# Kernel tuning notes

Measured on AMD Instinct MI355X. Metric: run time of the kernel, lower is better.

## Reference

```python
import jax, jax.numpy as jnp
import numpy as np

N_CHANNELS = 512
GROUPS = 8
EPS = 1e-5


def setup_inputs() -> dict:
    key = jax.random.key(0)
    ks = jax.random.split(key, 7)
    B, C, L = 8, N_CHANNELS, 4096
    s = 1.0 / np.sqrt(C)
    return {
        "x": jax.random.normal(ks[0], (B, C, L), dtype=jnp.float32),
        "gamma": jnp.ones((C,), dtype=jnp.float32),
        "beta": jnp.zeros((C,), dtype=jnp.float32),
        "w_qkv": jax.random.normal(ks[1], (3 * C, C), dtype=jnp.float32) * s,
        "b_qkv": jax.random.normal(ks[2], (3 * C,), dtype=jnp.float32) * 0.01,
        "w_out": jax.random.normal(ks[3], (C, C), dtype=jnp.float32) * s,
        "b_out": jax.random.normal(ks[4], (C,), dtype=jnp.float32) * 0.01,
    }


def group_norm(x, gamma, beta):
    # x: [B, C, L]; normalize per group of C//GROUPS channels over (channels_in_group, L)
    B, C, L = x.shape
    xg = x.reshape(B, GROUPS, C // GROUPS, L)
    mean = xg.mean(axis=(2, 3), keepdims=True)
    var = xg.var(axis=(2, 3), keepdims=True)
    xn = ((xg - mean) * jax.lax.rsqrt(var + EPS)).reshape(B, C, L)
    return xn * gamma[None, :, None] + beta[None, :, None]


def reference(x, gamma, beta, w_qkv, b_qkv, w_out, b_out):
    B, C, L = x.shape
    xn = group_norm(x, gamma, beta)
    # 1x1 conv == channel matmul: [3C, C] @ [B, C, L] -> [B, 3C, L]
    qkv = jnp.einsum('oc,bcl->bol', w_qkv, xn) + b_qkv[None, :, None]
    q, k, v = jnp.split(qkv, 3, axis=1)  # each [B, C, L]
    scale = C ** (-0.5)
    attn = jnp.einsum('bcl,bck->blk', q, k) * scale  # [B, L, L]
    attn = jax.nn.softmax(attn, axis=-1)
    out = jnp.einsum('blk,bck->bcl', attn, v)  # [B, C, L]
    proj = jnp.einsum('oc,bcl->bol', w_out, out) + b_out[None, :, None]
    return x + proj
```

## Files before the change

### kernel.cpp

```cpp
#include <hip/hip_runtime.h>

typedef __attribute__((ext_vector_type(4))) float f32x4;
typedef __attribute__((ext_vector_type(8))) short short8;
typedef unsigned short u16;
typedef unsigned int u32;

static constexpr int Bb = 8, Cc = 512, Ll = 4096;

__device__ __forceinline__ u16 f2bf(float f) {
  u32 u = __builtin_bit_cast(u32, f);
  u = (u + 0x7FFFu + ((u >> 16) & 1u)) >> 16;
  return (u16)u;
}

__device__ __forceinline__ void load_lds16(const void* g, void* l) {
  __builtin_amdgcn_global_load_lds((const __attribute__((address_space(1))) void*)g,
                                   (__attribute__((address_space(3))) void*)l,
                                   16, 0, 0);
}

__global__ void cvt_bf16_kernel(const float* __restrict__ src, u16* __restrict__ dst, int n) {
  int stride = gridDim.x * blockDim.x;
  for (int i = blockIdx.x * blockDim.x + threadIdx.x; i < n; i += stride)
    dst[i] = f2bf(src[i]);
}

__global__ __launch_bounds__(256)
void gn_stats_kernel(const float* __restrict__ x, float* __restrict__ stats) {
  int bg = blockIdx.x;
  const f32x4* p = (const f32x4*)(x + (size_t)bg * (64 * Ll));
  float s = 0.f, ss = 0.f;
  for (int i = threadIdx.x; i < 64 * Ll / 4; i += 256) {
    f32x4 v = p[i];
    s  += v[0] + v[1] + v[2] + v[3];
    ss += v[0]*v[0] + v[1]*v[1] + v[2]*v[2] + v[3]*v[3];
  }
  __shared__ float rs[256], rq[256];
  rs[threadIdx.x] = s; rq[threadIdx.x] = ss;
  __syncthreads();
  for (int st = 128; st > 0; st >>= 1) {
    if (threadIdx.x < st) { rs[threadIdx.x] += rs[threadIdx.x + st]; rq[threadIdx.x] += rq[threadIdx.x + st]; }
    __syncthreads();
  }
  if (threadIdx.x == 0) {
    const float inv_n = 1.f / (64.f * 4096.f);
    float mean = rs[0] * inv_n;
    float var  = rq[0] * inv_n - mean * mean;
    stats[bg * 2]     = mean;
    stats[bg * 2 + 1] = rsqrtf(var + 1e-5f);
  }
}

__global__ __launch_bounds__(256)
void gn_apply_t_kernel(const float* __restrict__ x, const float* __restrict__ gamma,
                       const float* __restrict__ beta, const float* __restrict__ stats,
                       u16* __restrict__ xn_t) {
  int lt = blockIdx.x;
  int ct = blockIdx.y;
  int b  = blockIdx.z;
  __shared__ float tile[64][65];
  int t = threadIdx.x;
  int lx = t & 63;
  int qd = t >> 6;
  int c0 = ct * 64, l0 = lt * 64;
  float mean = stats[(b * 8 + ct) * 2];
  float rstd = stats[(b * 8 + ct) * 2 + 1];
  #pragma unroll
  for (int i = 0; i < 16; ++i) {
    int cl = qd + i * 4;
    int c = c0 + cl;
    float v = x[((size_t)b * Cc + c) * Ll + l0 + lx];
    tile[cl][lx] = (v - mean) * rstd * gamma[c] + beta[c];
  }
  __syncthreads();
  #pragma unroll
  for (int i = 0; i < 16; ++i) {
    int ll = qd + i * 4;
    xn_t[((size_t)b * Ll + l0 + ll) * Cc + c0 + lx] = f2bf(tile[lx][ll]);
  }
}

template <int MODE>
__global__ __launch_bounds__(256, 2)
void gemm_tn(const u16* __restrict__ A, long long aStride, int lda,
             const u16* __restrict__ Bm, long long bStride, int ldb,
             void* __restrict__ Dv, long long dStride, int ldd,
             const float* __restrict__ bias, const float* __restrict__ resid, int K) {
  int z = blockIdx.z;
  A  += (size_t)z * aStride;
  Bm += (size_t)z * bStride;
  int m0 = blockIdx.x * 128, n0 = blockIdx.y * 128;
  __shared__ uint4 sA[1024], sB[1024];
  int tid = threadIdx.x, lane = tid & 63;
  int wv = tid >> 6, wr = wv >> 1, wc = wv & 1;
  int l15 = lane & 15, l4 = lane >> 4;
  f32x4 acc[4][4] = {};
  for (int kt = 0; kt < K; kt += 64) {
    __syncthreads();
    #pragma unroll
    for (int p = 0; p < 4; ++p) {
      int slot = p * 256 + tid;
      int r = slot >> 3, g = slot & 7, gw = g ^ (r & 7);
      load_lds16(A  + (size_t)(m0 + r) * lda + kt + gw * 8, &sA[slot]);
      load_lds16(Bm + (size_t)(n0 + r) * ldb + kt + gw * 8, &sB[slot]);
    }
    __syncthreads();
    #pragma unroll
    for (int ks = 0; ks < 2; ++ks) {
      short8 af[4], bfr[4];
      #pragma unroll
      for (int i = 0; i < 4; ++i) {
        int ra = 64 * wr + 16 * i + l15;
        af[i]  = *(const short8*)&sA[ra * 8 + ((4 * ks + l4) ^ (ra & 7))];
        int rb = 64 * wc + 16 * i + l15;
        bfr[i] = *(const short8*)&sB[rb * 8 + ((4 * ks + l4) ^ (rb & 7))];
      }
      #pragma unroll
      for (int i = 0; i < 4; ++i)
        #pragma unroll
        for (int j = 0; j < 4; ++j)
          acc[i][j] = __builtin_amdgcn_mfma_f32_16x16x32_bf16(af[i], bfr[j], acc[i][j], 0, 0, 0);
    }
  }
  #pragma unroll
  for (int i = 0; i < 4; ++i) {
    #pragma unroll
    for (int j = 0; j < 4; ++j) {
      #pragma unroll
      for (int r = 0; r < 4; ++r) {
        int m = m0 + 64 * wr + 16 * i + 4 * l4 + r;
        int n = n0 + 64 * wc + 16 * j + l15;
        float val = acc[i][j][r] + (MODE == 0 ? bias[n] : bias[m]);
        size_t idx = (size_t)z * dStride + (size_t)m * ldd + n;
        if (MODE == 2) ((float*)Dv)[idx] = val + resid[idx];
        else           ((u16*)Dv)[idx]   = f2bf(val);
      }
    }
  }
}

__global__ __launch_bounds__(512, 2)
void flash_attn_kernel(const u16* __restrict__ qk_t, const u16* __restrict__ v,
                       u16* __restrict__ o_t) {
  int b  = blockIdx.y;
  int q0 = blockIdx.x * 128;
  int tid = threadIdx.x, lane = tid & 63, wv = tid >> 6;
  int l15 = lane & 15, l4 = lane >> 4;
  const u16* qkb = qk_t + (size_t)b * Ll * 1024;
  const u16* vb  = v    + (size_t)b * Cc * Ll;
  u16* ob        = o_t  + (size_t)b * Ll * Cc;

  __shared__ uint4 sK[2][32 * 64];
  __shared__ uint4 sV[2][512 * 4];
  __shared__ __align__(16) char sP[128 * 80];
  __shared__ __align__(16) float sAl[128];

  int ow_q = wv >> 2, ow_c = wv & 3;

  short8 aq[16];
  {
    const u16* qp = qkb + (size_t)(q0 + wv * 16 + l15) * 1024 + 8 * l4;
    #pragma unroll
    for (int ks = 0; ks < 16; ++ks) aq[ks] = *(const short8*)(qp + 32 * ks);
  }

  auto issueK = [&](int kt, int buf) {
    #pragma unroll
    for (int p = 0; p < 4; ++p) {
      int slot = p * 512 + tid;
      int r = slot >> 6, g = slot & 63, gw = g ^ (r & 7);
      load_lds16(qkb + (size_t)(kt * 32 + r) * 1024 + 512 + gw * 8, &sK[buf][slot]);
    }
  };
  auto issueV = [&](int kt, int buf) {
    #pragma unroll
    for (int p = 0; p < 4; ++p) {
      int slot = p * 512 + tid;
      int r = slot >> 2, g = slot & 3, gw = g ^ ((r >> 1) & 3);
      load_lds16(vb + (size_t)r * Ll + kt * 32 + gw * 8, &sV[buf][slot]);
    }
  };
  issueK(0, 0);
  issueV(0, 0);

  f32x4 accO[4][8];
  #pragma unroll
  for (int i = 0; i < 4; ++i)
    #pragma unroll
    for (int j = 0; j < 8; ++j) accO[i][j] = (f32x4){0.f, 0.f, 0.f, 0.f};
  float mrun = -1e30f, lrun = 0.f;
  const float scale = 0.044194173824159216f;

  const int NT = Ll / 32;
  for (int kt = 0; kt < NT; ++kt) {
    int buf = kt & 1;
    __syncthreads();
    if (kt + 1 < NT) { issueK(kt + 1, buf ^ 1); issueV(kt + 1, buf ^ 1); }

    const uint4* kb = &sK[buf][0];
    f32x4 s2[2];
    #pragma unroll
    for (int t = 0; t < 2; ++t) {
      s2[t] = (f32x4){0.f, 0.f, 0.f, 0.f};
      int krow = 16 * t + l15;
      #pragma unroll
      for (int ks = 0; ks < 16; ++ks) {
        short8 ak = *(const short8*)&kb[krow * 64 + ((4 * ks + l4) ^ (krow & 7))];
        s2[t] = __builtin_amdgcn_mfma_f32_16x16x32_bf16(ak, aq[ks], s2[t], 0, 0, 0);
      }
    }

    #pragma unroll
    for (int t = 0; t < 2; ++t)
      #pragma unroll
      for (int r = 0; r < 4; ++r) s2[t][r] *= scale;
    float mx = fmaxf(fmaxf(s2[0][0], s2[0][1]), fmaxf(s2[0][2], s2[0][3]));
    mx = fmaxf(mx, fmaxf(fmaxf(s2[1][0], s2[1][1]), fmaxf(s2[1][2], s2[1][3])));
    mx = fmaxf(mx, __shfl_xor(mx, 16));
    mx = fmaxf(mx, __shfl_xor(mx, 32));
    float mnew = fmaxf(mrun, mx);
    float al = __expf(mrun - mnew);
    mrun = mnew;
    float ps = 0.f;
    #pragma unroll
    for (int t = 0; t < 2; ++t)
      #pragma unroll
      for (int r = 0; r < 4; ++r) { float pv = __expf(s2[t][r] - mnew); s2[t][r] = pv; ps += pv; }
    ps += __shfl_xor(ps, 16);
    ps += __shfl_xor(ps, 32);
    lrun = lrun * al + ps;

    {
      char* pb = sP + (16 * wv + l15) * 80;
      #pragma unroll
      for (int t = 0; t < 2; ++t) {
        u32 lo = (u32)f2bf(s2[t][0]) | ((u32)f2bf(s2[t][1]) << 16);
        u32 hi = (u32)f2bf(s2[t][2]) | ((u32)f2bf(s2[t][3]) << 16);
        uint2 w = {lo, hi};
        *(uint2*)(pb + 32 * t + 8 * l4) = w;
      }
      if (lane < 16) sAl[16 * wv + lane] = al;
    }

    __builtin_amdgcn_sched_barrier(0);
    asm volatile("s_waitcnt lgkmcnt(0)" ::: "memory");
    __builtin_amdgcn_s_barrier();
    __builtin_amdgcn_sched_barrier(0);

    #pragma unroll
    for (int i = 0; i < 4; ++i) {
      f32x4 av = *(const f32x4*)&sAl[64 * ow_q + 16 * i + 4 * l4];
      #pragma unroll
      for (int j = 0; j < 8; ++j) {
        #pragma unroll
        for (int r = 0; r < 4; ++r) accO[i][j][r] *= av[r];
      }
    }
    short8 ap[4];
    #pragma unroll
    for (int i = 0; i < 4; ++i) {
      int ra = 64 * ow_q + 16 * i + l15;
      ap[i] = *(const short8*)(sP + ra * 80 + 16 * l4);
    }
    const uint4* vbuf = &sV[buf][0];
    #pragma unroll
    for (int j = 0; j < 8; ++j) {
      int crow = 128 * ow_c + 16 * j + l15;
      short8 bv = *(const short8*)&vbuf[crow * 4 + (l4 ^ ((crow >> 1) & 3))];
      #pragma unroll
      for (int i = 0; i < 4; ++i)
        accO[i][j] = __builtin_amdgcn_mfma_f32_16x16x32_bf16(ap[i], bv, accO[i][j], 0, 0, 0);
    }
  }

  __syncthreads();
  if (lane < 16) sAl[16 * wv + lane] = lrun;
  __syncthreads();
  #pragma unroll
  for (int i = 0; i < 4; ++i) {
    f32x4 lv = *(const f32x4*)&sAl[64 * ow_q + 16 * i + 4 * l4];
    #pragma unroll
    for (int r = 0; r < 4; ++r) lv[r] = 1.f / lv[r];
    #pragma unroll
    for (int j = 0; j < 8; ++j) {
      #pragma unroll
      for (int r = 0; r < 4; ++r) {
        int q = q0 + 64 * ow_q + 16 * i + 4 * l4 + r;
        int c = 128 * ow_c + 16 * j + l15;
        ob[(size_t)q * Cc + c] = f2bf(accO[i][j][r] * lv[r]);
      }
    }
  }
}

extern "C" void kernel_launch(void* const* d_in, const int* in_sizes, int n_in,
                              void* d_out, int out_size, void* d_ws, size_t ws_size,
                              hipStream_t stream) {
  const float* x     = (const float*)d_in[0];
  const float* gamma = (const float*)d_in[1];
  const float* beta  = (const float*)d_in[2];
  const float* w_qkv = (const float*)d_in[3];
  const float* b_qkv = (const float*)d_in[4];
  const float* w_out = (const float*)d_in[5];
  const float* b_out = (const float*)d_in[6];
  float* out = (float*)d_out;

  char* ws = (char*)d_ws;
  size_t off = 0;
  auto alloc = [&](size_t bytes) -> char* {
    char* p = ws + off;
    off += (bytes + 1023) & ~(size_t)1023;
    return p;
  };
  float* stats = (float*)alloc(64 * 2 * sizeof(float));
  u16* wqb = (u16*)alloc((size_t)1536 * 512 * 2);
  u16* wob = (u16*)alloc((size_t)512 * 512 * 2);
  u16* xnt = (u16*)alloc((size_t)Bb * Ll * Cc * 2);
  u16* qkt = (u16*)alloc((size_t)Bb * Ll * 1024 * 2);
  u16* vbf = (u16*)alloc((size_t)Bb * Cc * Ll * 2);
  u16* ot  = xnt;
  if (off > ws_size) return;

  cvt_bf16_kernel<<<256, 256, 0, stream>>>(w_qkv, wqb, 1536 * 512);
  cvt_bf16_kernel<<<256, 256, 0, stream>>>(w_out, wob, 512 * 512);
  gn_stats_kernel<<<64, 256, 0, stream>>>(x, stats);
  gn_apply_t_kernel<<<dim3(64, 8, 8), 256, 0, stream>>>(x, gamma, beta, stats, xnt);
  gemm_tn<0><<<dim3(32, 8, 8), 256, 0, stream>>>(
      xnt, (long long)Ll * Cc, Cc, wqb, 0, Cc,
      qkt, (long long)Ll * 1024, 1024, b_qkv, nullptr, Cc);
  gemm_tn<1><<<dim3(4, 32, 8), 256, 0, stream>>>(
      wqb + (size_t)1024 * 512, 0, Cc, xnt, (long long)Ll * Cc, Cc,
      vbf, (long long)Cc * Ll, Ll, b_qkv + 1024, nullptr, Cc);
  flash_attn_kernel<<<dim3(32, 8), 512, 0, stream>>>(qkt, vbf, ot);
  gemm_tn<2><<<dim3(4, 32, 8), 256, 0, stream>>>(
      wob, 0, Cc, ot, (long long)Ll * Cc, Cc,
      out, (long long)Cc * Ll, Ll, b_out, x, Cc);
}
```

Measured before the change: 745.8 us.

## Replace XOR-swizzled LDS layouts with fragment-ordered tiles and interleave attention blocks across batches

The GEMM and flash-attention K tiles are now stored in LDS in MFMA fragment order instead of an XOR-swizzled row layout, so each wave's fragment reads hit contiguous addresses. This targets LDS bank conflicts and address arithmetic in the inner loops. The P scratch buffer row stride drops from 80 to 64 bytes, which may bring back bank conflicts on the P writes and reads. The attention grid is flattened so consecutive blocks cycle through batches, which changes how work and L2 traffic spread across CUs.

```diff
diff --git a/kernel.cpp b/kernel.cpp
--- a/kernel.cpp
+++ b/kernel.cpp
@@ -99,10 +99,11 @@
     __syncthreads();
     #pragma unroll
     for (int p = 0; p < 4; ++p) {
-      int slot = p * 256 + tid;
-      int r = slot >> 3, g = slot & 7, gw = g ^ (r & 7);
-      load_lds16(A  + (size_t)(m0 + r) * lda + kt + gw * 8, &sA[slot]);
-      load_lds16(Bm + (size_t)(n0 + r) * ldb + kt + gw * 8, &sB[slot]);
+      int s = p * 256 + tid;
+      int r = ((s >> 7) << 4) | (((s >> 2) & 1) << 3) | ((s >> 3) & 7);
+      int g = (((s >> 6) & 1) << 2) | (s & 3);
+      load_lds16(A  + (size_t)(m0 + r) * lda + kt + g * 8, &sA[s]);
+      load_lds16(Bm + (size_t)(n0 + r) * ldb + kt + g * 8, &sB[s]);
     }
     __syncthreads();
     #pragma unroll
@@ -110,10 +111,10 @@
       short8 af[4], bfr[4];
       #pragma unroll
       for (int i = 0; i < 4; ++i) {
-        int ra = 64 * wr + 16 * i + l15;
-        af[i]  = *(const short8*)&sA[ra * 8 + ((4 * ks + l4) ^ (ra & 7))];
-        int rb = 64 * wc + 16 * i + l15;
-        bfr[i] = *(const short8*)&sB[rb * 8 + ((4 * ks + l4) ^ (rb & 7))];
+        int sa = (4 * wr + i) * 128 + ks * 64 + (l15 & 7) * 8 + (l15 >> 3) * 4 + l4;
+        af[i]  = *(const short8*)&sA[sa];
+        int sb = (4 * wc + i) * 128 + ks * 64 + (l15 & 7) * 8 + (l15 >> 3) * 4 + l4;
+        bfr[i] = *(const short8*)&sB[sb];
       }
       #pragma unroll
       for (int i = 0; i < 4; ++i)
@@ -142,8 +143,9 @@
 __global__ __launch_bounds__(512, 2)
 void flash_attn_kernel(const u16* __restrict__ qk_t, const u16* __restrict__ v,
                        u16* __restrict__ o_t) {
-  int b  = blockIdx.y;
-  int q0 = blockIdx.x * 128;
+  int bid = blockIdx.x;
+  int b  = bid & 7;
+  int q0 = (bid >> 3) * 128;
   int tid = threadIdx.x, lane = tid & 63, wv = tid >> 6;
   int l15 = lane & 15, l4 = lane >> 4;
   const u16* qkb = qk_t + (size_t)b * Ll * 1024;
@@ -152,7 +154,7 @@
 
   __shared__ uint4 sK[2][32 * 64];
   __shared__ uint4 sV[2][512 * 4];
-  __shared__ __align__(16) char sP[128 * 80];
+  __shared__ __align__(16) char sP[128 * 64];
   __shared__ __align__(16) float sAl[128];
 
   int ow_q = wv >> 2, ow_c = wv & 3;
@@ -167,17 +169,18 @@
   auto issueK = [&](int kt, int buf) {
     #pragma unroll
     for (int p = 0; p < 4; ++p) {
-      int slot = p * 512 + tid;
-      int r = slot >> 6, g = slot & 63, gw = g ^ (r & 7);
-      load_lds16(qkb + (size_t)(kt * 32 + r) * 1024 + 512 + gw * 8, &sK[buf][slot]);
+      int s = p * 512 + tid;
+      int kr = (((s >> 6) & 1) << 4) | (((s >> 2) & 1) << 3) | ((s >> 3) & 7);
+      int g  = ((s >> 7) << 2) | (s & 3);
+      load_lds16(qkb + (size_t)(kt * 32 + kr) * 1024 + 512 + g * 8, &sK[buf][s]);
     }
   };
   auto issueV = [&](int kt, int buf) {
     #pragma unroll
     for (int p = 0; p < 4; ++p) {
-      int slot = p * 512 + tid;
-      int r = slot >> 2, g = slot & 3, gw = g ^ ((r >> 1) & 3);
-      load_lds16(vb + (size_t)r * Ll + kt * 32 + gw * 8, &sV[buf][slot]);
+      int s = p * 512 + tid;
+      int r = s >> 2, g = s & 3, gw = g ^ ((r >> 1) & 3);
+      load_lds16(vb + (size_t)r * Ll + kt * 32 + gw * 8, &sV[buf][s]);
     }
   };
   issueK(0, 0);
@@ -202,10 +205,9 @@
     #pragma unroll
     for (int t = 0; t < 2; ++t) {
       s2[t] = (f32x4){0.f, 0.f, 0.f, 0.f};
-      int krow = 16 * t + l15;
       #pragma unroll
       for (int ks = 0; ks < 16; ++ks) {
-        short8 ak = *(const short8*)&kb[krow * 64 + ((4 * ks + l4) ^ (krow & 7))];
+        short8 ak = *(const short8*)&kb[ks * 128 + t * 64 + (l15 & 7) * 8 + (l15 >> 3) * 4 + l4];
         s2[t] = __builtin_amdgcn_mfma_f32_16x16x32_bf16(ak, aq[ks], s2[t], 0, 0, 0);
       }
     }
@@ -231,7 +233,7 @@
     lrun = lrun * al + ps;
 
     {
-      char* pb = sP + (16 * wv + l15) * 80;
+      char* pb = sP + (16 * wv + l15) * 64;
       #pragma unroll
       for (int t = 0; t < 2; ++t) {
         u32 lo = (u32)f2bf(s2[t][0]) | ((u32)f2bf(s2[t][1]) << 16);
@@ -260,7 +262,7 @@
     #pragma unroll
     for (int i = 0; i < 4; ++i) {
       int ra = 64 * ow_q + 16 * i + l15;
-      ap[i] = *(const short8*)(sP + ra * 80 + 16 * l4);
+      ap[i] = *(const short8*)(sP + ra * 64 + 16 * l4);
     }
     const uint4* vbuf = &sV[buf][0];
     #pragma unroll
@@ -331,7 +333,7 @@
   gemm_tn<1><<<dim3(4, 32, 8), 256, 0, stream>>>(
       wqb + (size_t)1024 * 512, 0, Cc, xnt, (long long)Ll * Cc, Cc,
       vbf, (long long)Cc * Ll, Ll, b_qkv + 1024, nullptr, Cc);
-  flash_attn_kernel<<<dim3(32, 8), 512, 0, stream>>>(qkt, vbf, ot);
+  flash_attn_kernel<<<256, 512, 0, stream>>>(qkt, vbf, ot);
   gemm_tn<2><<<dim3(4, 32, 8), 256, 0, stream>>>(
       wob, 0, Cc, ot, (long long)Ll * Cc, Cc,
       out, (long long)Cc * Ll, Ll, b_out, x, Cc);
```

Result: faster. 684.6 us (-8.2%).
